# Kernel tuning notes

Hardware: AMD Instinct MI355X
Metric: run time of the kernel (lower is better)

## Reference

```python
import jax, jax.numpy as jnp
import numpy as np

N = 50000      # nodes
E = 400000     # edges (before self loops)
IN = 128       # in_feat
HID = 64       # n_hidden per head
HEADS = [4, 4, 1]
NEG_SLOPE = 0.2  # DGL GATConv default


def gat_layer(h, src, dst, W, al, ar, b, n_nodes):
    # h: [N, Din]; W: [Din, H*F]; al/ar: [H, F]; b: [H*F]
    H, F = al.shape
    feat = (h @ W).reshape(n_nodes, H, F)              # [N,H,F]
    el = jnp.sum(feat * al, axis=-1)                   # [N,H]
    er = jnp.sum(feat * ar, axis=-1)                   # [N,H]
    e = jax.nn.leaky_relu(el[src] + er[dst], NEG_SLOPE)  # [E,H]
    # edge softmax over destination node segments (stable)
    e_max = jax.lax.stop_gradient(jax.ops.segment_max(e, dst, num_segments=n_nodes))
    ex = jnp.exp(e - e_max[dst])                       # [E,H]
    denom = jax.ops.segment_sum(ex, dst, num_segments=n_nodes)  # [N,H]
    alpha = ex / denom[dst]                            # [E,H]
    msg = feat[src] * alpha[:, :, None]                # [E,H,F]
    out = jax.ops.segment_sum(msg, dst, num_segments=n_nodes)   # [N,H,F]
    out = out + b.reshape(1, H, F)
    return out.reshape(n_nodes, H * F)


def setup_inputs() -> dict:
    key = jax.random.key(0)
    ks = jax.random.split(key, 16)
    inp = {
        "node_feat": jax.random.normal(ks[0], (N, IN), jnp.float32),
        "src": jax.random.randint(ks[1], (E,), 0, N),
        "dst": jax.random.randint(ks[2], (E,), 0, N),
    }
    dins = [IN, HID * HEADS[0], HID * HEADS[1]]
    for i, (din, h) in enumerate(zip(dins, HEADS)):
        k = 3 + 3 * i
        inp[f"W{i}"] = jax.random.normal(ks[k], (din, h * HID), jnp.float32) * 0.1
        inp[f"al{i}"] = jax.random.normal(ks[k + 1], (h, HID), jnp.float32) * 0.1
        inp[f"ar{i}"] = jax.random.normal(ks[k + 2], (h, HID), jnp.float32) * 0.1
        inp[f"b{i}"] = jnp.zeros((h * HID,), jnp.float32)
    return inp


def reference(node_feat, src, dst, W0, al0, ar0, b0, W1, al1, ar1, b1, W2, al2, ar2, b2):
    n_nodes = node_feat.shape[0]
    # add_self_loop
    loop = jnp.arange(n_nodes, dtype=src.dtype)
    src_a = jnp.concatenate([src, loop])
    dst_a = jnp.concatenate([dst, loop])
    h = node_feat
    h = gat_layer(h, src_a, dst_a, W0, al0, ar0, b0, n_nodes)  # [N, 4*64]
    h = gat_layer(h, src_a, dst_a, W1, al1, ar1, b1, n_nodes)  # [N, 4*64]
    h = gat_layer(h, src_a, dst_a, W2, al2, ar2, b2, n_nodes)  # [N, 64]
    return h
```

## Files before the change

### kernel.cpp

```cpp
#include <hip/hip_runtime.h>


typedef __attribute__((ext_vector_type(8))) short short8;
typedef __attribute__((ext_vector_type(4))) float f32x4;

__device__ __forceinline__ float bf2f(ushort u) {
  union { unsigned int i; float f; } c;
  c.i = ((unsigned int)u) << 16;
  return c.f;
}
__device__ __forceinline__ ushort f2bf(float f) {
  union { float f; unsigned int i; } c;
  c.f = f;
  unsigned int u = c.i;
  u += 0x7FFFu + ((u >> 16) & 1u);
  return (ushort)(u >> 16);
}
__device__ __forceinline__ float lrelu_exp(float x) {
  const float y = fmaxf(x, 0.2f * x);
  return __expf(y);
}
__device__ __forceinline__ void gload_lds16(const ushort* g, void* lds) {
  __builtin_amdgcn_global_load_lds(
      (const __attribute__((address_space(1))) unsigned int*)g,
      (__attribute__((address_space(3))) unsigned int*)lds, 16, 0, 0);
}

__global__ __launch_bounds__(256) void prep_kernel(
    const float* __restrict__ nf, ushort* __restrict__ a0, int n8, int nbA,
    const float* __restrict__ W0, ushort* __restrict__ Wt0,
    const float* __restrict__ W1, ushort* __restrict__ Wt1,
    const float* __restrict__ W2, ushort* __restrict__ Wt2) {
  const int b = blockIdx.x;
  if (b < nbA) {
    const int i = b * 256 + threadIdx.x;
    if (i >= n8) return;
    const float4 v0 = ((const float4*)nf)[i * 2];
    const float4 v1 = ((const float4*)nf)[i * 2 + 1];
    short8 o;
    o[0] = (short)f2bf(v0.x); o[1] = (short)f2bf(v0.y);
    o[2] = (short)f2bf(v0.z); o[3] = (short)f2bf(v0.w);
    o[4] = (short)f2bf(v1.x); o[5] = (short)f2bf(v1.y);
    o[6] = (short)f2bf(v1.z); o[7] = (short)f2bf(v1.w);
    ((short8*)a0)[i] = o;
  } else {
    const int i = (b - nbA) * 256 + threadIdx.x;
    if (i < 32768) {
      const int k = i >> 8, n = i & 255;
      Wt0[n * 128 + k] = f2bf(W0[i]);
    } else if (i < 32768 + 65536) {
      const int j = i - 32768;
      const int k = j >> 8, n = j & 255;
      Wt1[n * 256 + k] = f2bf(W1[j]);
    } else if (i < 32768 + 65536 + 16384) {
      const int j = i - 32768 - 65536;
      const int k = j >> 6, n = j & 63;
      Wt2[n * 256 + k] = f2bf(W2[j]);
    }
  }
}

template <int BN>
__global__ __launch_bounds__(256) void gemm_mfma(
    const ushort* __restrict__ A, const ushort* __restrict__ Wt,
    ushort* __restrict__ C, int M, int K, int Nc) {
  constexpr int NF = BN / 32;
  constexpr int NCHB = BN / 8;
  __shared__ ushort As[128][64];
  __shared__ ushort Bs[BN][64];
  const int bm = blockIdx.x * 128;
  const int bn = blockIdx.y * BN;
  const int tid = threadIdx.x;
  const int lane = tid & 63;
  const int wave = tid >> 6;
  const int wm = wave >> 1;
  const int wn = wave & 1;
  const int lrow = lane >> 3;
  const int lslot = lane & 7;

  f32x4 acc[4][NF];
#pragma unroll
  for (int m = 0; m < 4; ++m)
#pragma unroll
    for (int n = 0; n < NF; ++n) acc[m][n] = 0.f;

  for (int k0 = 0; k0 < K; k0 += 64) {
#pragma unroll
    for (int c = wave; c < 16; c += 4) {
      const int row = c * 8 + lrow;
      int rg = bm + row;
      if (rg >= M) rg = M - 1;
      const int kcol = (lslot ^ (row & 7)) * 8;
      gload_lds16(A + (size_t)rg * K + k0 + kcol,
                  (char*)(&As[0][0]) + c * 1024 + lrow * 128 + lslot * 16);
    }
#pragma unroll
    for (int c = wave; c < NCHB; c += 4) {
      const int row = c * 8 + lrow;
      const int kcol = (lslot ^ (row & 7)) * 8;
      gload_lds16(Wt + (size_t)(bn + row) * K + k0 + kcol,
                  (char*)(&Bs[0][0]) + c * 1024 + lrow * 128 + lslot * 16);
    }
    __syncthreads();

#pragma unroll
    for (int kk = 0; kk < 2; ++kk) {
      short8 a[4], b[NF];
#pragma unroll
      for (int m = 0; m < 4; ++m) {
        const int row = wm * 64 + m * 16 + (lane & 15);
        const int slot = (kk * 4 + (lane >> 4)) ^ (row & 7);
        a[m] = *(const short8*)((const char*)&As[0][0] + row * 128 + slot * 16);
      }
#pragma unroll
      for (int n = 0; n < NF; ++n) {
        const int row = wn * (NF * 16) + n * 16 + (lane & 15);
        const int slot = (kk * 4 + (lane >> 4)) ^ (row & 7);
        b[n] = *(const short8*)((const char*)&Bs[0][0] + row * 128 + slot * 16);
      }
#pragma unroll
      for (int m = 0; m < 4; ++m)
#pragma unroll
        for (int n = 0; n < NF; ++n)
          acc[m][n] = __builtin_amdgcn_mfma_f32_16x16x32_bf16(
              a[m], b[n], acc[m][n], 0, 0, 0);
    }
    __syncthreads();
  }

#pragma unroll
  for (int m = 0; m < 4; ++m) {
#pragma unroll
    for (int r = 0; r < 4; ++r) {
      const int row = bm + wm * 64 + m * 16 + (lane >> 4) * 4 + r;
      if (row < M) {
#pragma unroll
        for (int n = 0; n < NF; ++n) {
          const int col = bn + wn * (NF * 16) + n * 16 + (lane & 15);
          C[(size_t)row * Nc + col] = f2bf(acc[m][n][r]);
        }
      }
    }
  }
}

__global__ __launch_bounds__(256) void attn_coef_h4(
    const ushort* __restrict__ feat, const float* __restrict__ al,
    const float* __restrict__ ar, float* __restrict__ el,
    float* __restrict__ er, int Nn) {
  if (blockIdx.x == 0 && threadIdx.x < 4) el[Nn * 4 + threadIdx.x] = -1e9f;
  const int n = (blockIdx.x * 256 + threadIdx.x) >> 6;
  const int lane = threadIdx.x & 63;
  if (n >= Nn) return;
  const short4 v = ((const short4*)(feat + (size_t)n * 256))[lane];
  const float4 a = ((const float4*)al)[lane];
  const float4 r = ((const float4*)ar)[lane];
  const float f0 = bf2f((ushort)v.x), f1 = bf2f((ushort)v.y),
              f2 = bf2f((ushort)v.z), f3 = bf2f((ushort)v.w);
  float pl = f0 * a.x + f1 * a.y + f2 * a.z + f3 * a.w;
  float pr = f0 * r.x + f1 * r.y + f2 * r.z + f3 * r.w;
#pragma unroll
  for (int off = 1; off < 16; off <<= 1) {
    pl += __shfl_xor(pl, off);
    pr += __shfl_xor(pr, off);
  }
  if ((lane & 15) == 0) {
    el[n * 4 + (lane >> 4)] = pl;
    er[n * 4 + (lane >> 4)] = pr;
  }
}

__global__ __launch_bounds__(256) void attn_coef_h1(
    const ushort* __restrict__ feat, const float* __restrict__ al,
    const float* __restrict__ ar, float* __restrict__ el,
    float* __restrict__ er, int Nn) {
  if (blockIdx.x == 0 && threadIdx.x == 0) el[Nn] = -1e9f;
  const int wid = (blockIdx.x * 256 + threadIdx.x) >> 6;
  const int lane = threadIdx.x & 63;
  const int n = wid * 4 + (lane >> 4);
  const int sub = lane & 15;
  if (n >= Nn) return;
  const short4 v = ((const short4*)(feat + (size_t)n * 64))[sub];
  const float4 a = ((const float4*)al)[sub];
  const float4 r = ((const float4*)ar)[sub];
  const float f0 = bf2f((ushort)v.x), f1 = bf2f((ushort)v.y),
              f2 = bf2f((ushort)v.z), f3 = bf2f((ushort)v.w);
  float pl = f0 * a.x + f1 * a.y + f2 * a.z + f3 * a.w;
  float pr = f0 * r.x + f1 * r.y + f2 * r.z + f3 * r.w;
#pragma unroll
  for (int off = 1; off < 16; off <<= 1) {
    pl += __shfl_xor(pl, off);
    pr += __shfl_xor(pr, off);
  }
  if (sub == 0) {
    el[n] = pl;
    er[n] = pr;
  }
}

__global__ void hist_kernel(const int* __restrict__ dst, int* __restrict__ cnt,
                            int E, int Nn) {
  const int e = blockIdx.x * blockDim.x + threadIdx.x;
  if (e >= E + Nn) return;
  const int d = (e < E) ? dst[e] : (e - E);
  atomicAdd(&cnt[d], 1);
}

__device__ __forceinline__ int block_incl_scan_1024(int x, int* lds16) {
  const int lane = threadIdx.x & 63;
  const int wid = threadIdx.x >> 6;
  int inc = x;
#pragma unroll
  for (int off = 1; off < 64; off <<= 1) {
    const int y = __shfl_up(inc, off);
    if (lane >= off) inc += y;
  }
  if (lane == 63) lds16[wid] = inc;
  __syncthreads();
  if (wid == 0) {
    int t = (lane < 16) ? lds16[lane] : 0;
#pragma unroll
    for (int off = 1; off < 16; off <<= 1) {
      const int y = __shfl_up(t, off);
      if (lane >= off) t += y;
    }
    if (lane < 16) lds16[lane] = t;
  }
  __syncthreads();
  if (wid > 0) inc += lds16[wid - 1];
  return inc;
}

__global__ __launch_bounds__(1024) void scan_blocks_kernel(
    const int* __restrict__ cnt, int* __restrict__ row_ptr,
    int* __restrict__ partials, int n) {
  __shared__ int lds16[16];
  const int i = blockIdx.x * 1024 + threadIdx.x;
  const int x = (i < n) ? ((cnt[i] + 3) & ~3) : 0;
  const int inc = block_incl_scan_1024(x, lds16);
  if (i < n) row_ptr[i] = inc - x;
  if (threadIdx.x == 1023) partials[blockIdx.x] = inc;
}

__global__ __launch_bounds__(1024) void scan_partials_kernel(
    int* __restrict__ partials, int* __restrict__ row_ptr, int nb, int n) {
  __shared__ int lds16[16];
  const int x = (threadIdx.x < nb) ? partials[threadIdx.x] : 0;
  const int inc = block_incl_scan_1024(x, lds16);
  if (threadIdx.x < nb) partials[threadIdx.x] = inc - x;
  if (threadIdx.x == nb - 1) row_ptr[n] = inc;
}

__global__ __launch_bounds__(1024) void add_offsets_kernel(
    int* __restrict__ row_ptr, int* __restrict__ cursor,
    const int* __restrict__ partials, int n) {
  const int i = blockIdx.x * 1024 + threadIdx.x;
  if (i < n) {
    const int v = row_ptr[i] + partials[blockIdx.x];
    row_ptr[i] = v;
    cursor[i] = v;
  }
}

__global__ void scatter_kernel(const int* __restrict__ src,
                               const int* __restrict__ dst,
                               int* __restrict__ cursor, int* __restrict__ esrc,
                               int E, int Nn) {
  const int e = blockIdx.x * blockDim.x + threadIdx.x;
  if (e >= E + Nn) return;
  const int s = (e < E) ? src[e] : (e - E);
  const int d = (e < E) ? dst[e] : (e - E);
  const int pos = atomicAdd(&cursor[d], 1);
  esrc[pos] = s;
}

__global__ void fill_pad_kernel(const int* __restrict__ cursor,
                                const int* __restrict__ row_ptr,
                                int* __restrict__ esrc, int Nn) {
  const int n = blockIdx.x * 256 + threadIdx.x;
  if (n >= Nn) return;
  const int end = row_ptr[n + 1];
  for (int p = cursor[n]; p < end; ++p) esrc[p] = Nn;
}

__global__ __launch_bounds__(256) void agg_fused_h4(
    const int* __restrict__ row_ptr, const int* __restrict__ esrc,
    const float* __restrict__ el, const float* __restrict__ er,
    const ushort* __restrict__ feat, const float* __restrict__ b,
    ushort* __restrict__ out, int Nn) {
  const int n = (blockIdx.x * 256 + threadIdx.x) >> 6;
  const int lane = threadIdx.x & 63;
  if (n >= Nn) return;
  const int h = lane >> 4;
  int i = row_ptr[n];
  const int end = row_ptr[n + 1];
  const float erv = er[n * 4 + h];
  const short4* fb = (const short4*)feat + lane;

  float den = 0.f;
  f32x4 acc = 0.f;
  int s0 = esrc[i], s1 = esrc[i + 1], s2 = esrc[i + 2], s3 = esrc[i + 3];
  float x0 = el[s0 * 4 + h], x1 = el[s1 * 4 + h], x2 = el[s2 * 4 + h],
        x3 = el[s3 * 4 + h];
  short4 f0 = fb[(size_t)s0 * 64], f1 = fb[(size_t)s1 * 64],
         f2 = fb[(size_t)s2 * 64], f3 = fb[(size_t)s3 * 64];
  for (i += 4; i < end; i += 4) {
    const int t0 = esrc[i], t1 = esrc[i + 1], t2 = esrc[i + 2],
              t3 = esrc[i + 3];
    const float y0 = el[t0 * 4 + h], y1 = el[t1 * 4 + h], y2 = el[t2 * 4 + h],
                y3 = el[t3 * 4 + h];
    const short4 g0 = fb[(size_t)t0 * 64], g1 = fb[(size_t)t1 * 64],
                 g2 = fb[(size_t)t2 * 64], g3 = fb[(size_t)t3 * 64];
    const float e0 = lrelu_exp(x0 + erv), e1 = lrelu_exp(x1 + erv),
                e2 = lrelu_exp(x2 + erv), e3 = lrelu_exp(x3 + erv);
    den += (e0 + e1) + (e2 + e3);
    acc[0] += e0 * bf2f((ushort)f0.x) + e1 * bf2f((ushort)f1.x) +
              e2 * bf2f((ushort)f2.x) + e3 * bf2f((ushort)f3.x);
    acc[1] += e0 * bf2f((ushort)f0.y) + e1 * bf2f((ushort)f1.y) +
              e2 * bf2f((ushort)f2.y) + e3 * bf2f((ushort)f3.y);
    acc[2] += e0 * bf2f((ushort)f0.z) + e1 * bf2f((ushort)f1.z) +
              e2 * bf2f((ushort)f2.z) + e3 * bf2f((ushort)f3.z);
    acc[3] += e0 * bf2f((ushort)f0.w) + e1 * bf2f((ushort)f1.w) +
              e2 * bf2f((ushort)f2.w) + e3 * bf2f((ushort)f3.w);
    x0 = y0; x1 = y1; x2 = y2; x3 = y3;
    f0 = g0; f1 = g1; f2 = g2; f3 = g3;
  }
  {
    const float e0 = lrelu_exp(x0 + erv), e1 = lrelu_exp(x1 + erv),
                e2 = lrelu_exp(x2 + erv), e3 = lrelu_exp(x3 + erv);
    den += (e0 + e1) + (e2 + e3);
    acc[0] += e0 * bf2f((ushort)f0.x) + e1 * bf2f((ushort)f1.x) +
              e2 * bf2f((ushort)f2.x) + e3 * bf2f((ushort)f3.x);
    acc[1] += e0 * bf2f((ushort)f0.y) + e1 * bf2f((ushort)f1.y) +
              e2 * bf2f((ushort)f2.y) + e3 * bf2f((ushort)f3.y);
    acc[2] += e0 * bf2f((ushort)f0.z) + e1 * bf2f((ushort)f1.z) +
              e2 * bf2f((ushort)f2.z) + e3 * bf2f((ushort)f3.z);
    acc[3] += e0 * bf2f((ushort)f0.w) + e1 * bf2f((ushort)f1.w) +
              e2 * bf2f((ushort)f2.w) + e3 * bf2f((ushort)f3.w);
  }
  const float rden = 1.f / den;
  const float4 bb = ((const float4*)b)[lane];
  short4 o;
  o.x = (short)f2bf(acc[0] * rden + bb.x);
  o.y = (short)f2bf(acc[1] * rden + bb.y);
  o.z = (short)f2bf(acc[2] * rden + bb.z);
  o.w = (short)f2bf(acc[3] * rden + bb.w);
  ((short4*)out)[(size_t)n * 64 + lane] = o;
}

__global__ __launch_bounds__(256) void agg_fused_h1(
    const int* __restrict__ row_ptr, const int* __restrict__ esrc,
    const float* __restrict__ el, const float* __restrict__ er,
    const ushort* __restrict__ feat, const float* __restrict__ b,
    float* __restrict__ out, int Nn) {
  const int wid = (blockIdx.x * 256 + threadIdx.x) >> 6;
  const int lane = threadIdx.x & 63;
  const int n = wid * 2 + (lane >> 5);
  const int sub = lane & 31;
  if (n >= Nn) return;
  int i = row_ptr[n];
  const int end = row_ptr[n + 1];
  const float erv = er[n];
  const uint* fb = (const uint*)feat + sub;

  float den = 0.f;
  float a0 = 0.f, a1 = 0.f;
  int s0 = esrc[i], s1 = esrc[i + 1], s2 = esrc[i + 2], s3 = esrc[i + 3];
  float x0 = el[s0], x1 = el[s1], x2 = el[s2], x3 = el[s3];
  uint f0 = fb[(size_t)s0 * 32], f1 = fb[(size_t)s1 * 32],
       f2 = fb[(size_t)s2 * 32], f3 = fb[(size_t)s3 * 32];
  for (i += 4; i < end; i += 4) {
    const int t0 = esrc[i], t1 = esrc[i + 1], t2 = esrc[i + 2],
              t3 = esrc[i + 3];
    const float y0 = el[t0], y1 = el[t1], y2 = el[t2], y3 = el[t3];
    const uint g0 = fb[(size_t)t0 * 32], g1 = fb[(size_t)t1 * 32],
               g2 = fb[(size_t)t2 * 32], g3 = fb[(size_t)t3 * 32];
    const float e0 = lrelu_exp(x0 + erv), e1 = lrelu_exp(x1 + erv),
                e2 = lrelu_exp(x2 + erv), e3 = lrelu_exp(x3 + erv);
    den += (e0 + e1) + (e2 + e3);
    a0 += e0 * bf2f((ushort)(f0 & 0xffff)) + e1 * bf2f((ushort)(f1 & 0xffff)) +
          e2 * bf2f((ushort)(f2 & 0xffff)) + e3 * bf2f((ushort)(f3 & 0xffff));
    a1 += e0 * bf2f((ushort)(f0 >> 16)) + e1 * bf2f((ushort)(f1 >> 16)) +
          e2 * bf2f((ushort)(f2 >> 16)) + e3 * bf2f((ushort)(f3 >> 16));
    x0 = y0; x1 = y1; x2 = y2; x3 = y3;
    f0 = g0; f1 = g1; f2 = g2; f3 = g3;
  }
  {
    const float e0 = lrelu_exp(x0 + erv), e1 = lrelu_exp(x1 + erv),
                e2 = lrelu_exp(x2 + erv), e3 = lrelu_exp(x3 + erv);
    den += (e0 + e1) + (e2 + e3);
    a0 += e0 * bf2f((ushort)(f0 & 0xffff)) + e1 * bf2f((ushort)(f1 & 0xffff)) +
          e2 * bf2f((ushort)(f2 & 0xffff)) + e3 * bf2f((ushort)(f3 & 0xffff));
    a1 += e0 * bf2f((ushort)(f0 >> 16)) + e1 * bf2f((ushort)(f1 >> 16)) +
          e2 * bf2f((ushort)(f2 >> 16)) + e3 * bf2f((ushort)(f3 >> 16));
  }
  const float rden = 1.f / den;
  const float2 bb = ((const float2*)b)[sub];
  float2 o;
  o.x = a0 * rden + bb.x;
  o.y = a1 * rden + bb.y;
  ((float2*)out)[(size_t)n * 32 + sub] = o;
}

static void run_layer(const ushort* hin, int K, int H, const ushort* Wt,
                      const float* al, const float* ar, const float* b,
                      ushort* feat, void* out, float* el, float* er,
                      const int* row_ptr, const int* esrc, int Nn,
                      hipStream_t stream) {
  const int HF = H * 64;
  if (H == 4) {
    dim3 gg((Nn + 127) / 128, HF / 128);
    gemm_mfma<128><<<gg, 256, 0, stream>>>(hin, Wt, feat, Nn, K, HF);
    const int waves_grid = (Nn * 64 + 255) / 256;
    attn_coef_h4<<<waves_grid, 256, 0, stream>>>(feat, al, ar, el, er, Nn);
    agg_fused_h4<<<waves_grid, 256, 0, stream>>>(row_ptr, esrc, el, er, feat,
                                                 b, (ushort*)out, Nn);
  } else {
    dim3 gg((Nn + 127) / 128, HF / 64);
    gemm_mfma<64><<<gg, 256, 0, stream>>>(hin, Wt, feat, Nn, K, HF);
    attn_coef_h1<<<(Nn * 16 + 255) / 256, 256, 0, stream>>>(feat, al, ar, el,
                                                            er, Nn);
    agg_fused_h1<<<(Nn * 32 + 255) / 256, 256, 0, stream>>>(
        row_ptr, esrc, el, er, feat, b, (float*)out, Nn);
  }
}

extern "C" void kernel_launch(void* const* d_in, const int* in_sizes, int n_in,
                              void* d_out, int out_size, void* d_ws,
                              size_t ws_size, hipStream_t stream) {
  const float* nf = (const float*)d_in[0];
  const int* src = (const int*)d_in[1];
  const int* dst = (const int*)d_in[2];
  const float* W0 = (const float*)d_in[3];
  const float* al0 = (const float*)d_in[4];
  const float* ar0 = (const float*)d_in[5];
  const float* b0 = (const float*)d_in[6];
  const float* W1 = (const float*)d_in[7];
  const float* al1 = (const float*)d_in[8];
  const float* ar1 = (const float*)d_in[9];
  const float* b1 = (const float*)d_in[10];
  const float* W2 = (const float*)d_in[11];
  const float* al2 = (const float*)d_in[12];
  const float* ar2 = (const float*)d_in[13];
  const float* b2 = (const float*)d_in[14];

  const int IN = 128;
  const int Nn = in_sizes[0] / IN;
  const int E = in_sizes[1];
  const int ETP = E + 4 * Nn;

  char* ws = (char*)d_ws;
  size_t off = 0;
  auto alloc = [&](size_t bytes) {
    char* p = ws + off;
    off += (bytes + 255) & ~(size_t)255;
    return p;
  };
  ushort* feat = (ushort*)alloc(((size_t)Nn + 1) * 256 * 2);
  ushort* h1 = (ushort*)alloc((size_t)Nn * 256 * 2);
  ushort* h2 = (ushort*)alloc((size_t)Nn * 256 * 2);
  ushort* a0 = (ushort*)alloc((size_t)Nn * 128 * 2);
  ushort* Wt0 = (ushort*)alloc((size_t)256 * 128 * 2);
  ushort* Wt1 = (ushort*)alloc((size_t)256 * 256 * 2);
  ushort* Wt2 = (ushort*)alloc((size_t)64 * 256 * 2);
  float* el = (float*)alloc(((size_t)Nn + 1) * 4 * 4);
  float* er = (float*)alloc((size_t)Nn * 4 * 4);
  int* row_ptr = (int*)alloc(((size_t)Nn + 1) * 4);
  int* cnt = (int*)alloc((size_t)Nn * 4);
  int* cursor = (int*)alloc((size_t)Nn * 4);
  int* esrc = (int*)alloc((size_t)ETP * 4);
  int* partials = (int*)alloc((size_t)1024 * 4);
  (void)ws_size;
  (void)n_in;
  (void)out_size;

  hipMemsetAsync(feat + (size_t)Nn * 256, 0, 512, stream);

  const int n8 = Nn * 16;
  const int nbA = (n8 + 255) / 256;
  const int nbB = (32768 + 65536 + 16384 + 255) / 256;
  prep_kernel<<<nbA + nbB, 256, 0, stream>>>(nf, a0, n8, nbA, W0, Wt0, W1, Wt1,
                                             W2, Wt2);

  const int ET = E + Nn;
  const int nb = (Nn + 1023) / 1024;
  hipMemsetAsync(cnt, 0, (size_t)Nn * sizeof(int), stream);
  hist_kernel<<<(ET + 255) / 256, 256, 0, stream>>>(dst, cnt, E, Nn);
  scan_blocks_kernel<<<nb, 1024, 0, stream>>>(cnt, row_ptr, partials, Nn);
  scan_partials_kernel<<<1, 1024, 0, stream>>>(partials, row_ptr, nb, Nn);
  add_offsets_kernel<<<nb, 1024, 0, stream>>>(row_ptr, cursor, partials, Nn);
  scatter_kernel<<<(ET + 255) / 256, 256, 0, stream>>>(src, dst, cursor, esrc,
                                                       E, Nn);
  fill_pad_kernel<<<(Nn + 255) / 256, 256, 0, stream>>>(cursor, row_ptr, esrc,
                                                        Nn);

  run_layer(a0, IN, 4, Wt0, al0, ar0, b0, feat, h1, el, er, row_ptr, esrc, Nn,
            stream);
  run_layer(h1, 256, 4, Wt1, al1, ar1, b1, feat, h2, el, er, row_ptr, esrc, Nn,
            stream);
  run_layer(h2, 256, 1, Wt2, al2, ar2, b2, feat, d_out, el, er, row_ptr, esrc,
            Nn, stream);
}
```

Baseline: 224.8 us.

## Fuse attention coefficient computation into GEMM epilogue and fold memsets into prep

For the two 4-head layers, the el/er attention dot products are now computed in the MFMA GEMM epilogue from fp32 accumulators, removing the separate attn_coef_h4 kernel and its re-read of the feature matrix. The two hipMemsetAsync calls and the sentinel writes move into extra blocks of the prep kernel, cutting launch count. The fused epilogue uses unrounded accumulators rather than bf16-rounded features, which changes numerics slightly, and it adds shuffle reductions and register pressure to the GEMM.

```diff
diff --git a/kernel.cpp b/kernel.cpp
--- a/kernel.cpp
+++ b/kernel.cpp
@@ -3,6 +3,7 @@
 
 typedef __attribute__((ext_vector_type(8))) short short8;
 typedef __attribute__((ext_vector_type(4))) float f32x4;
+typedef __attribute__((ext_vector_type(4))) int int4v;
 
 __device__ __forceinline__ float bf2f(ushort u) {
   union { unsigned int i; float f; } c;
@@ -30,7 +31,9 @@
     const float* __restrict__ nf, ushort* __restrict__ a0, int n8, int nbA,
     const float* __restrict__ W0, ushort* __restrict__ Wt0,
     const float* __restrict__ W1, ushort* __restrict__ Wt1,
-    const float* __restrict__ W2, ushort* __restrict__ Wt2) {
+    const float* __restrict__ W2, ushort* __restrict__ Wt2, int nbW,
+    int* __restrict__ cnt, int Nn, int nbZ, ushort* __restrict__ feat_sent,
+    float* __restrict__ el4, float* __restrict__ el1) {
   const int b = blockIdx.x;
   if (b < nbA) {
     const int i = b * 256 + threadIdx.x;
@@ -43,7 +46,7 @@
     o[4] = (short)f2bf(v1.x); o[5] = (short)f2bf(v1.y);
     o[6] = (short)f2bf(v1.z); o[7] = (short)f2bf(v1.w);
     ((short8*)a0)[i] = o;
-  } else {
+  } else if (b < nbA + nbW) {
     const int i = (b - nbA) * 256 + threadIdx.x;
     if (i < 32768) {
       const int k = i >> 8, n = i & 255;
@@ -57,13 +60,28 @@
       const int k = j >> 6, n = j & 63;
       Wt2[n * 256 + k] = f2bf(W2[j]);
     }
-  }
-}
-
-template <int BN>
+  } else if (b < nbA + nbW + nbZ) {
+    const int idx = (b - nbA - nbW) * 256 + threadIdx.x;
+    const int base = idx * 4;
+    if (base + 4 <= Nn) {
+      ((int4v*)cnt)[idx] = (int4v)0;
+    } else if (base < Nn) {
+      for (int j = base; j < Nn; ++j) cnt[j] = 0;
+    }
+  } else {
+    const int t = threadIdx.x;
+    if (t < 128) ((uint*)feat_sent)[t] = 0u;
+    if (t >= 128 && t < 132) el4[(size_t)Nn * 4 + (t - 128)] = -1e9f;
+    if (t == 132) el1[Nn] = -1e9f;
+  }
+}
+
+template <int BN, bool FUSE>
 __global__ __launch_bounds__(256) void gemm_mfma(
     const ushort* __restrict__ A, const ushort* __restrict__ Wt,
-    ushort* __restrict__ C, int M, int K, int Nc) {
+    ushort* __restrict__ C, int M, int K, int Nc,
+    const float* __restrict__ al, const float* __restrict__ ar,
+    float* __restrict__ el, float* __restrict__ er) {
   constexpr int NF = BN / 32;
   constexpr int NCHB = BN / 8;
   __shared__ ushort As[128][64];
@@ -142,31 +160,40 @@
       }
     }
   }
-}
-
-__global__ __launch_bounds__(256) void attn_coef_h4(
-    const ushort* __restrict__ feat, const float* __restrict__ al,
-    const float* __restrict__ ar, float* __restrict__ el,
-    float* __restrict__ er, int Nn) {
-  if (blockIdx.x == 0 && threadIdx.x < 4) el[Nn * 4 + threadIdx.x] = -1e9f;
-  const int n = (blockIdx.x * 256 + threadIdx.x) >> 6;
-  const int lane = threadIdx.x & 63;
-  if (n >= Nn) return;
-  const short4 v = ((const short4*)(feat + (size_t)n * 256))[lane];
-  const float4 a = ((const float4*)al)[lane];
-  const float4 r = ((const float4*)ar)[lane];
-  const float f0 = bf2f((ushort)v.x), f1 = bf2f((ushort)v.y),
-              f2 = bf2f((ushort)v.z), f3 = bf2f((ushort)v.w);
-  float pl = f0 * a.x + f1 * a.y + f2 * a.z + f3 * a.w;
-  float pr = f0 * r.x + f1 * r.y + f2 * r.z + f3 * r.w;
-#pragma unroll
-  for (int off = 1; off < 16; off <<= 1) {
-    pl += __shfl_xor(pl, off);
-    pr += __shfl_xor(pr, off);
-  }
-  if ((lane & 15) == 0) {
-    el[n * 4 + (lane >> 4)] = pl;
-    er[n * 4 + (lane >> 4)] = pr;
+
+  if constexpr (FUSE) {
+    const int cc = lane & 15;
+    const int head = blockIdx.y * 2 + wn;
+    float alv[NF], arv[NF];
+#pragma unroll
+    for (int n = 0; n < NF; ++n) {
+      alv[n] = al[head * 64 + n * 16 + cc];
+      arv[n] = ar[head * 64 + n * 16 + cc];
+    }
+#pragma unroll
+    for (int m = 0; m < 4; ++m) {
+#pragma unroll
+      for (int r = 0; r < 4; ++r) {
+        float pl = 0.f, pr = 0.f;
+#pragma unroll
+        for (int n = 0; n < NF; ++n) {
+          pl = fmaf(acc[m][n][r], alv[n], pl);
+          pr = fmaf(acc[m][n][r], arv[n], pr);
+        }
+#pragma unroll
+        for (int o = 1; o < 16; o <<= 1) {
+          pl += __shfl_xor(pl, o);
+          pr += __shfl_xor(pr, o);
+        }
+        if (cc == 0) {
+          const int row = bm + wm * 64 + m * 16 + (lane >> 4) * 4 + r;
+          if (row < M) {
+            el[row * 4 + head] = pl;
+            er[row * 4 + head] = pr;
+          }
+        }
+      }
+    }
   }
 }
 
@@ -174,7 +201,6 @@
     const ushort* __restrict__ feat, const float* __restrict__ al,
     const float* __restrict__ ar, float* __restrict__ el,
     float* __restrict__ er, int Nn) {
-  if (blockIdx.x == 0 && threadIdx.x == 0) el[Nn] = -1e9f;
   const int wid = (blockIdx.x * 256 + threadIdx.x) >> 6;
   const int lane = threadIdx.x & 63;
   const int n = wid * 4 + (lane >> 4);
@@ -402,29 +428,6 @@
   ((float2*)out)[(size_t)n * 32 + sub] = o;
 }
 
-static void run_layer(const ushort* hin, int K, int H, const ushort* Wt,
-                      const float* al, const float* ar, const float* b,
-                      ushort* feat, void* out, float* el, float* er,
-                      const int* row_ptr, const int* esrc, int Nn,
-                      hipStream_t stream) {
-  const int HF = H * 64;
-  if (H == 4) {
-    dim3 gg((Nn + 127) / 128, HF / 128);
-    gemm_mfma<128><<<gg, 256, 0, stream>>>(hin, Wt, feat, Nn, K, HF);
-    const int waves_grid = (Nn * 64 + 255) / 256;
-    attn_coef_h4<<<waves_grid, 256, 0, stream>>>(feat, al, ar, el, er, Nn);
-    agg_fused_h4<<<waves_grid, 256, 0, stream>>>(row_ptr, esrc, el, er, feat,
-                                                 b, (ushort*)out, Nn);
-  } else {
-    dim3 gg((Nn + 127) / 128, HF / 64);
-    gemm_mfma<64><<<gg, 256, 0, stream>>>(hin, Wt, feat, Nn, K, HF);
-    attn_coef_h1<<<(Nn * 16 + 255) / 256, 256, 0, stream>>>(feat, al, ar, el,
-                                                            er, Nn);
-    agg_fused_h1<<<(Nn * 32 + 255) / 256, 256, 0, stream>>>(
-        row_ptr, esrc, el, er, feat, b, (float*)out, Nn);
-  }
-}
-
 extern "C" void kernel_launch(void* const* d_in, const int* in_sizes, int n_in,
                               void* d_out, int out_size, void* d_ws,
                               size_t ws_size, hipStream_t stream) {
@@ -463,8 +466,10 @@
   ushort* Wt0 = (ushort*)alloc((size_t)256 * 128 * 2);
   ushort* Wt1 = (ushort*)alloc((size_t)256 * 256 * 2);
   ushort* Wt2 = (ushort*)alloc((size_t)64 * 256 * 2);
-  float* el = (float*)alloc(((size_t)Nn + 1) * 4 * 4);
-  float* er = (float*)alloc((size_t)Nn * 4 * 4);
+  float* el4 = (float*)alloc(((size_t)Nn + 1) * 4 * 4);
+  float* er4 = (float*)alloc((size_t)Nn * 4 * 4);
+  float* el1 = (float*)alloc(((size_t)Nn + 1) * 4);
+  float* er1 = (float*)alloc((size_t)Nn * 4);
   int* row_ptr = (int*)alloc(((size_t)Nn + 1) * 4);
   int* cnt = (int*)alloc((size_t)Nn * 4);
   int* cursor = (int*)alloc((size_t)Nn * 4);
@@ -474,17 +479,16 @@
   (void)n_in;
   (void)out_size;
 
-  hipMemsetAsync(feat + (size_t)Nn * 256, 0, 512, stream);
-
   const int n8 = Nn * 16;
   const int nbA = (n8 + 255) / 256;
-  const int nbB = (32768 + 65536 + 16384 + 255) / 256;
-  prep_kernel<<<nbA + nbB, 256, 0, stream>>>(nf, a0, n8, nbA, W0, Wt0, W1, Wt1,
-                                             W2, Wt2);
+  const int nbW = (32768 + 65536 + 16384 + 255) / 256;
+  const int nbZ = (Nn + 1023) / 1024;
+  prep_kernel<<<nbA + nbW + nbZ + 1, 256, 0, stream>>>(
+      nf, a0, n8, nbA, W0, Wt0, W1, Wt1, W2, Wt2, nbW, cnt, Nn, nbZ,
+      feat + (size_t)Nn * 256, el4, el1);
 
   const int ET = E + Nn;
   const int nb = (Nn + 1023) / 1024;
-  hipMemsetAsync(cnt, 0, (size_t)Nn * sizeof(int), stream);
   hist_kernel<<<(ET + 255) / 256, 256, 0, stream>>>(dst, cnt, E, Nn);
   scan_blocks_kernel<<<nb, 1024, 0, stream>>>(cnt, row_ptr, partials, Nn);
   scan_partials_kernel<<<1, 1024, 0, stream>>>(partials, row_ptr, nb, Nn);
@@ -494,10 +498,30 @@
   fill_pad_kernel<<<(Nn + 255) / 256, 256, 0, stream>>>(cursor, row_ptr, esrc,
                                                         Nn);
 
-  run_layer(a0, IN, 4, Wt0, al0, ar0, b0, feat, h1, el, er, row_ptr, esrc, Nn,
-            stream);
-  run_layer(h1, 256, 4, Wt1, al1, ar1, b1, feat, h2, el, er, row_ptr, esrc, Nn,
-            stream);
-  run_layer(h2, 256, 1, Wt2, al2, ar2, b2, feat, d_out, el, er, row_ptr, esrc,
-            Nn, stream);
-}
+  const int waves_grid = (Nn * 64 + 255) / 256;
+
+  {
+    dim3 gg((Nn + 127) / 128, 2);
+    gemm_mfma<128, true><<<gg, 256, 0, stream>>>(a0, Wt0, feat, Nn, 128, 256,
+                                                 al0, ar0, el4, er4);
+    agg_fused_h4<<<waves_grid, 256, 0, stream>>>(row_ptr, esrc, el4, er4, feat,
+                                                 b0, h1, Nn);
+  }
+  {
+    dim3 gg((Nn + 127) / 128, 2);
+    gemm_mfma<128, true><<<gg, 256, 0, stream>>>(h1, Wt1, feat, Nn, 256, 256,
+                                                 al1, ar1, el4, er4);
+    agg_fused_h4<<<waves_grid, 256, 0, stream>>>(row_ptr, esrc, el4, er4, feat,
+                                                 b1, h2, Nn);
+  }
+  {
+    dim3 gg((Nn + 127) / 128, 1);
+    gemm_mfma<64, false><<<gg, 256, 0, stream>>>(h2, Wt2, feat, Nn, 256, 64,
+                                                 nullptr, nullptr, nullptr,
+                                                 nullptr);
+    attn_coef_h1<<<(Nn * 16 + 255) / 256, 256, 0, stream>>>(feat, al2, ar2,
+                                                            el1, er1, Nn);
+    agg_fused_h1<<<(Nn * 32 + 255) / 256, 256, 0, stream>>>(
+        row_ptr, esrc, el1, er1, feat, b2, (float*)d_out, Nn);
+  }
+}
```

Result: faster. 211.8 us (-5.8%).
